# Kernel tuning notes

Hardware: AMD Instinct MI355X
Metric: run time of the kernel (lower is better)

## Reference

```python
import jax, jax.numpy as jnp
import numpy as np

B, S, D = 2, 2048, 2048
H, HK = 16, 4          # n_heads, n_kv_heads
DK = D // H            # 128
REP = H // HK


def setup_inputs() -> dict:
    key = jax.random.key(0)
    ks = jax.random.split(key, 9)
    x = jax.random.normal(ks[0], (B, S, D), dtype=jnp.float32)
    # RoPE tables: [max_seq_len, d_k/2]
    inv_freq = 1.0 / (10000.0 ** (jnp.arange(0, DK, 2, dtype=jnp.float32) / DK))
    t = jnp.arange(S, dtype=jnp.float32)
    freqs = jnp.outer(t, inv_freq)  # [S, DK/2]
    freqs_cos = jnp.cos(freqs)
    freqs_sin = jnp.sin(freqs)
    sc = 0.02
    return {
        "x": x,
        "freqs_cos": freqs_cos,
        "freqs_sin": freqs_sin,
        "wq_w": jax.random.normal(ks[1], (D, D), dtype=jnp.float32) * sc,
        "wq_b": jnp.zeros((D,), dtype=jnp.float32),
        "wk_w": jax.random.normal(ks[2], (HK * DK, D), dtype=jnp.float32) * sc,
        "wk_b": jnp.zeros((HK * DK,), dtype=jnp.float32),
        "wv_w": jax.random.normal(ks[3], (HK * DK, D), dtype=jnp.float32) * sc,
        "wv_b": jnp.zeros((HK * DK,), dtype=jnp.float32),
        "wo_w": jax.random.normal(ks[4], (D, D), dtype=jnp.float32) * sc,
        "wo_b": jnp.zeros((D,), dtype=jnp.float32),
    }


def _apply_rope(t, cos, sin):
    # t: [b, h, s, dk]; cos/sin: [1, 1, s, dk/2]; interleaved pairs (even=real, odd=imag)
    tr = t[..., 0::2]
    ti = t[..., 1::2]
    out_r = tr * cos - ti * sin
    out_i = tr * sin + ti * cos
    return jnp.stack([out_r, out_i], axis=-1).reshape(t.shape)


def reference(x, freqs_cos, freqs_sin, wq_w, wq_b, wk_w, wk_b, wv_w, wv_b, wo_w, wo_b):
    b, s, d = x.shape
    q = (x @ wq_w.T + wq_b).reshape(b, s, H, DK).transpose(0, 2, 1, 3)   # [b,H,s,dk]
    k = (x @ wk_w.T + wk_b).reshape(b, s, HK, DK).transpose(0, 2, 1, 3)  # [b,HK,s,dk]
    v = (x @ wv_w.T + wv_b).reshape(b, s, HK, DK).transpose(0, 2, 1, 3)

    cos = freqs_cos[:s][None, None]  # [1,1,s,dk/2]
    sin = freqs_sin[:s][None, None]
    q = _apply_rope(q, cos, sin)
    k = _apply_rope(k, cos, sin)

    # GQA: group q heads by kv head instead of materializing repeat_kv
    qg = q.reshape(b, HK, REP, s, DK)
    scores = jnp.einsum("bgrqd,bgkd->bgrqk", qg, k) / jnp.sqrt(jnp.float32(DK))
    causal = jnp.triu(jnp.full((s, s), -jnp.inf, dtype=scores.dtype), k=1)
    attn = jax.nn.softmax(scores + causal, axis=-1)  # dropout=0.0 -> no-op
    out = jnp.einsum("bgrqk,bgkd->bgrqd", attn, v)   # [b,HK,REP,s,dk]
    out = out.reshape(b, H, s, DK).transpose(0, 2, 1, 3).reshape(b, s, d)
    return out @ wo_w.T + wo_b
```

## Files before the change

### kernel.cpp

```cpp
#include <hip/hip_runtime.h>

#define BDIM 2
#define SDIM 2048
#define DDIM 2048
#define HQ 16
#define HKV 4
#define DKH 128
#define NKV 512
#define NQKV 3072
#define MROWS 4096

typedef __attribute__((ext_vector_type(8))) short bf16x8;
typedef __attribute__((ext_vector_type(4))) float f32x4;
typedef __attribute__((ext_vector_type(8))) unsigned short u16x8;
typedef __attribute__((ext_vector_type(4))) unsigned short u16x4;

#define AS1 __attribute__((address_space(1)))
#define AS3 __attribute__((address_space(3)))

__device__ __forceinline__ unsigned short f2bf(float f) {
    union { float f; unsigned int u; } v; v.f = f;
    unsigned int r = v.u + 0x7FFFu + ((v.u >> 16) & 1u);
    return (unsigned short)(r >> 16);
}
__device__ __forceinline__ float bf2f(unsigned short u) {
    union { unsigned int u; float f; } v; v.u = ((unsigned int)u) << 16;
    return v.f;
}
__device__ __forceinline__ unsigned int pack2bf(float a, float b) {
    return (unsigned int)f2bf(a) | ((unsigned int)f2bf(b) << 16);
}

#define NX   ((size_t)MROWS * DDIM)
#define NWQ  ((size_t)DDIM * DDIM)
#define NWKV ((size_t)NKV * DDIM)
#define CAST_BLOCKS 18432
__global__ void cast_all(const float* __restrict__ x, const float* __restrict__ wq,
                         const float* __restrict__ wk, const float* __restrict__ wv,
                         const float* __restrict__ wo, unsigned short* __restrict__ dst,
                         const float* __restrict__ qb, const float* __restrict__ kb,
                         const float* __restrict__ vb, float* __restrict__ b3) {
    if (blockIdx.x >= CAST_BLOCKS) {
        int i = (blockIdx.x - CAST_BLOCKS) * 256 + threadIdx.x;
        if (i < DDIM) b3[i] = qb[i];
        else if (i < DDIM + NKV) b3[i] = kb[i - DDIM];
        else if (i < NQKV) b3[i] = vb[i - DDIM - NKV];
        return;
    }
    size_t i = ((size_t)blockIdx.x * blockDim.x + threadIdx.x) * 4;
    const size_t N0 = NX, N1 = N0 + NWQ, N2 = N1 + NWKV, N3 = N2 + NWKV;
    const float* src; size_t off;
    if (i < N0)      { src = x;  off = i; }
    else if (i < N1) { src = wq; off = i - N0; }
    else if (i < N2) { src = wk; off = i - N1; }
    else if (i < N3) { src = wv; off = i - N2; }
    else             { src = wo; off = i - N3; }
    float4 v = *(const float4*)(src + off);
    u16x4 o;
    o[0] = f2bf(v.x); o[1] = f2bf(v.y); o[2] = f2bf(v.z); o[3] = f2bf(v.w);
    *(u16x4*)(dst + i) = o;
}

__global__ void rope_trans(unsigned short* __restrict__ buf,
                           const float* __restrict__ cosT, const float* __restrict__ sinT,
                           unsigned short* __restrict__ Vt, float qscale) {
    if (blockIdx.x < MROWS) {
        int r = blockIdx.x, pos = r & (SDIM - 1);
        int col0 = threadIdx.x * 8;
        unsigned short* p = buf + (size_t)r * NQKV + col0;
        int i0 = (col0 & 127) >> 1;
        float4 c4 = *(const float4*)(cosT + pos * 64 + i0);
        float4 s4 = *(const float4*)(sinT + pos * 64 + i0);
        float sc = (col0 < DDIM) ? qscale : 1.f;
        u16x8 v = *(const u16x8*)p;
        u16x8 o;
        float cc[4] = {c4.x, c4.y, c4.z, c4.w}, ss[4] = {s4.x, s4.y, s4.z, s4.w};
#pragma unroll
        for (int k = 0; k < 4; ++k) {
            float xr = bf2f(v[2 * k]), xi = bf2f(v[2 * k + 1]);
            o[2 * k]     = f2bf((xr * cc[k] - xi * ss[k]) * sc);
            o[2 * k + 1] = f2bf((xr * ss[k] + xi * cc[k]) * sc);
        }
        *(u16x8*)p = o;
    } else {
        __shared__ unsigned short T[32][33];
        if (threadIdx.x >= 256) return;
        int t = blockIdx.x - MROWS;
        int s0 = (t & 63) * 32, d0 = ((t >> 6) & 15) * 32, b = t >> 10;
        int c = threadIdx.x & 31, r4 = threadIdx.x >> 5;
        for (int rr = r4; rr < 32; rr += 8)
            T[rr][c] = buf[(size_t)(b * SDIM + s0 + rr) * NQKV + (DDIM + NKV) + d0 + c];
        __syncthreads();
        int cp = ((c & 0x0C) << 1) | ((c & 0x10) >> 2) | (c & 3);
        for (int rr = r4; rr < 32; rr += 8)
            Vt[(size_t)(b * NKV + d0 + rr) * SDIM + s0 + cp] = T[c][rr];
    }
}

template <int BF16OUT, int BM, int BN, int WM, int WN>
__global__ __launch_bounds__(512, 2) void gemm8(
    const unsigned short* __restrict__ A,
    const unsigned short* __restrict__ Bm,
    const float* __restrict__ bias,
    void* __restrict__ Cv,
    int pitch, int Kdim) {
    constexpr int NFRAG = BN / WN / 16;
    constexpr int AH = BM / 128;
    constexpr int BH = BN / 128;
    constexpr int AHR = BM / 2;
    constexpr int BHR = BN / 2;

    __shared__ unsigned short As[2][2][AHR * 64];
    __shared__ unsigned short Bs[2][2][BHR * 64];

    const int tid = threadIdx.x;
    const int lane = tid & 63;
    const int wid = tid >> 6;
    const int ml = lane & 15, quad = lane >> 4;
    const int wm = wid / WN, wn = wid % WN;
    const int bhf = wn / (WN / 2);
    const int brb = (wn % (WN / 2)) * (BN / WN);

    const int gx = gridDim.x;
    const int nwg = gx * gridDim.y;
    int w0 = blockIdx.y * gx + blockIdx.x;
    int wsw = (nwg & 7) ? w0 : ((w0 & 7) * (nwg >> 3) + (w0 >> 3));
    const int m0 = (wsw / gx) * BM, n0 = (wsw % gx) * BN;

    const int NT = Kdim >> 6;
    const int xr = ml & 7;

    const int sr = tid >> 3;
    const int sk = ((tid & 7) ^ (sr & 7)) * 8;
    const unsigned short* Ag0 = A + (size_t)(m0 + sr) * Kdim + sk;
    const unsigned short* Bg0 = Bm + (size_t)(n0 + sr) * Kdim + sk;

    f32x4 acc[8][NFRAG] = {};

#define STG_A(bf, hf, kt)                                                                       \
    do {                                                                                        \
        _Pragma("unroll")                                                                       \
        for (int ll = 0; ll < AH; ++ll)                                                         \
            __builtin_amdgcn_global_load_lds(                                                   \
                (const AS1 unsigned int*)(Ag0 + (size_t)((hf) * AHR + ll * 64) * Kdim + (kt)),  \
                (AS3 unsigned int*)(&As[bf][hf][ll * 4096 + tid * 8]), 16, 0, 0);               \
    } while (0)
#define STG_B(bf, hf, kt)                                                                       \
    do {                                                                                        \
        _Pragma("unroll")                                                                       \
        for (int ll = 0; ll < BH; ++ll)                                                         \
            __builtin_amdgcn_global_load_lds(                                                   \
                (const AS1 unsigned int*)(Bg0 + (size_t)((hf) * BHR + ll * 64) * Kdim + (kt)),  \
                (AS3 unsigned int*)(&Bs[bf][hf][ll * 4096 + tid * 8]), 16, 0, 0);               \
    } while (0)

    STG_B(0, 0, 0); STG_B(0, 1, 0);
    STG_A(0, 0, 0); STG_A(0, 1, 0);
    if (NT > 1) {
        STG_B(1, 0, 64); STG_B(1, 1, 64);
        if constexpr (BH == 1)      asm volatile("s_waitcnt vmcnt(2)" ::: "memory");
        else if constexpr (BH == 2) asm volatile("s_waitcnt vmcnt(4)" ::: "memory");
        else                        asm volatile("s_waitcnt vmcnt(6)" ::: "memory");
    } else {
        asm volatile("s_waitcnt vmcnt(0)" ::: "memory");
    }
    __builtin_amdgcn_s_barrier();

    for (int G = 0; G < NT; ++G) {
        const int cur = G & 1, nxt = cur ^ 1;
        const int ktA = (G + 1) * 64, ktB = (G + 2) * 64;
        const unsigned short* Bh = Bs[cur][bhf];

        bf16x8 bfr[NFRAG][2];
#pragma unroll
        for (int nj = 0; nj < NFRAG; ++nj)
#pragma unroll
            for (int kk = 0; kk < 2; ++kk)
                bfr[nj][kk] = *(const bf16x8*)&Bh[(brb + nj * 16 + ml) * 64 + ((kk * 4 + quad) ^ xr) * 8];

#pragma unroll
        for (int p = 0; p < 4; ++p) {
            bf16x8 af[2][2];
#pragma unroll
            for (int mi = 0; mi < 2; ++mi) {
                const int arow0 = wm * 128 + (p * 2 + mi) * 16;
                const int ahf = arow0 / AHR;
                const int arin = arow0 % AHR + ml;
#pragma unroll
                for (int kk = 0; kk < 2; ++kk)
                    af[mi][kk] = *(const bf16x8*)&As[cur][ahf][arin * 64 + ((kk * 4 + quad) ^ xr) * 8];
            }

            if (p == 0) {
                if (G + 1 < NT) { STG_A(nxt, 0, ktA); STG_A(nxt, 1, ktA); }
            } else if (p == 2) {
                if (G + 2 < NT) STG_B(cur, 0, ktB);
            } else if (p == 3) {
                if (G + 2 < NT) STG_B(cur, 1, ktB);
            }

            __builtin_amdgcn_s_barrier();
            __builtin_amdgcn_s_setprio(1);
#pragma unroll
            for (int kk = 0; kk < 2; ++kk)
#pragma unroll
                for (int mi = 0; mi < 2; ++mi)
#pragma unroll
                    for (int nj = 0; nj < NFRAG; ++nj)
                        acc[p * 2 + mi][nj] = __builtin_amdgcn_mfma_f32_16x16x32_bf16(
                            af[mi][kk], bfr[nj][kk], acc[p * 2 + mi][nj], 0, 0, 0);
            __builtin_amdgcn_s_setprio(0);
            if (p == 3) {
                if (G < NT - 2) {
                    if constexpr (BH == 1)      asm volatile("s_waitcnt vmcnt(2)" ::: "memory");
                    else if constexpr (BH == 2) asm volatile("s_waitcnt vmcnt(4)" ::: "memory");
                    else                        asm volatile("s_waitcnt vmcnt(6)" ::: "memory");
                } else if (G == NT - 2) {
                    asm volatile("s_waitcnt vmcnt(0)" ::: "memory");
                }
            }
            __builtin_amdgcn_s_barrier();
        }
    }
#undef STG_A
#undef STG_B

#pragma unroll
    for (int nj = 0; nj < NFRAG; ++nj) {
        const int col = n0 + wn * (BN / WN) + nj * 16 + ml;
        const float bj = bias[col];
#pragma unroll
        for (int mi = 0; mi < 8; ++mi) {
            const int row0 = m0 + wm * 128 + mi * 16 + quad * 4;
#pragma unroll
            for (int rr = 0; rr < 4; ++rr) {
                float v = acc[mi][nj][rr] + bj;
                if (BF16OUT)
                    ((unsigned short*)Cv)[(size_t)(row0 + rr) * pitch + col] = f2bf(v);
                else
                    ((float*)Cv)[(size_t)(row0 + rr) * pitch + col] = v;
            }
        }
    }
}

__global__ __launch_bounds__(256, 2) void attn_fwd(
    const unsigned short* __restrict__ Qp,
    const unsigned short* __restrict__ Kp,
    const unsigned short* __restrict__ Vt,
    unsigned short* __restrict__ O) {
    const int l = blockIdx.x;
    const int j = l & 15;
    const int h = (l >> 4) & 15;
    const int b = l >> 8;
    const int g = h >> 2;
    const int jh = 31 - j;
    const int tid = threadIdx.x;
    const int w = tid >> 6, lane = tid & 63;
    const int ml = lane & 15, quad = lane >> 4;
    const int rsub = lane >> 2, seg = lane & 3;
    const int pr = w >> 1;
    const int wsub = w & 1;

    __shared__ unsigned short Ks[2][4 * 64 * 32];
    __shared__ unsigned short Vs[2][2 * 128 * 32];

    int myqt = pr ? j : jh;
    int q0 = myqt * 64 + wsub * 32;

    bf16x8 aq[2][4];
    auto load_q = [&](int qt) {
#pragma unroll
        for (int g2 = 0; g2 < 2; ++g2) {
            const size_t qrow = (size_t)(b * SDIM + qt * 64 + wsub * 32 + g2 * 16 + ml);
#pragma unroll
            for (int kc = 0; kc < 4; ++kc)
                aq[g2][kc] = *(const bf16x8*)(Qp + qrow * NQKV + h * DKH + kc * 32 + quad * 8);
        }
    };
    load_q(myqt);

    f32x4 o_acc[2][8] = {};
    float l_acc[2] = {0.f, 0.f};

    auto store_out = [&](int qt) {
#pragma unroll
        for (int g2 = 0; g2 < 2; ++g2) {
            float lt = l_acc[g2];
            lt += __shfl_xor(lt, 16);
            lt += __shfl_xor(lt, 32);
            float inv = 1.f / lt;
            size_t rowbase = (size_t)(b * SDIM + qt * 64 + wsub * 32 + g2 * 16 + ml) * DDIM + h * DKH + quad * 4;
#pragma unroll
            for (int dt = 0; dt < 8; ++dt) {
                u16x4 ov;
#pragma unroll
                for (int r = 0; r < 4; ++r)
                    ov[r] = f2bf(o_acc[g2][dt][r] * inv);
                *(u16x4*)(O + rowbase + dt * 16) = ov;
            }
        }
    };

    for (int it = 0; it < 17; ++it) {
        int kt;
        if (pr == 0)       kt = it;
        else if (it <= j)  kt = it;
        else if (it <= 15) kt = 16 + it - j;
        else               kt = -1;

        __syncthreads();
        if (kt >= 0) {
            const int kb = kt * 64;
#pragma unroll
            for (int kc = 0; kc < 4; ++kc)
#pragma unroll
                for (int rh = 0; rh < 2; ++rh)
                    __builtin_amdgcn_global_load_lds(
                        (const AS1 unsigned int*)(Kp + (size_t)(b * SDIM + kb + rh * 32 + wsub * 16 + rsub) * NQKV + g * DKH + kc * 32 + seg * 8),
                        (AS3 unsigned int*)(&Ks[pr][kc * 2048 + rh * 1024 + wsub * 512 + lane * 8]), 16, 0, 0);
#pragma unroll
            for (int c = 0; c < 8; ++c) {
                int u = wsub * 8 + c, kc2 = u >> 3, rg = u & 7;
                __builtin_amdgcn_global_load_lds(
                    (const AS1 unsigned int*)(Vt + (size_t)(b * NKV + g * DKH + rg * 16 + rsub) * SDIM + kb + kc2 * 32 + seg * 8),
                    (AS3 unsigned int*)(&Vs[pr][u * 512 + lane * 8]), 16, 0, 0);
            }
        }
        __syncthreads();

        if (pr == 1 && it == j + 1) {
            store_out(j);
            myqt = jh; q0 = myqt * 64 + wsub * 32;
            load_q(jh);
#pragma unroll
            for (int g2 = 0; g2 < 2; ++g2) {
                l_acc[g2] = 0.f;
#pragma unroll
                for (int dt = 0; dt < 8; ++dt) o_acc[g2][dt] = (f32x4){0.f, 0.f, 0.f, 0.f};
            }
        }

        if (kt >= 0) {
            const int kb = kt * 64;
            __builtin_amdgcn_s_setprio(1);
            f32x4 st[2][4];
#pragma unroll
            for (int t = 0; t < 4; ++t) {
                bf16x8 ak[4];
#pragma unroll
                for (int kc = 0; kc < 4; ++kc)
                    ak[kc] = *(const bf16x8*)&Ks[pr][kc * 2048 + (t * 16 + ml) * 32 + quad * 8];
#pragma unroll
                for (int g2 = 0; g2 < 2; ++g2) {
                    f32x4 sc = {};
#pragma unroll
                    for (int kc = 0; kc < 4; ++kc)
                        sc = __builtin_amdgcn_mfma_f32_16x16x32_bf16(ak[kc], aq[g2][kc], sc, 0, 0, 0);
                    st[g2][t] = sc;
                }
            }

            if (kb + 63 > q0) {
#pragma unroll
                for (int g2 = 0; g2 < 2; ++g2) {
                    int qg = q0 + g2 * 16 + ml;
#pragma unroll
                    for (int t = 0; t < 4; ++t) {
                        int kvb = kb + t * 16 + quad * 4;
#pragma unroll
                        for (int r = 0; r < 4; ++r)
                            if (kvb + r > qg) st[g2][t][r] = -INFINITY;
                    }
                }
            }

            unsigned int pk[2][4][2];
#pragma unroll
            for (int g2 = 0; g2 < 2; ++g2) {
#pragma unroll
                for (int t = 0; t < 4; ++t) {
                    float p0 = __expf(st[g2][t][0] - 20.f);
                    float p1 = __expf(st[g2][t][1] - 20.f);
                    float p2 = __expf(st[g2][t][2] - 20.f);
                    float p3 = __expf(st[g2][t][3] - 20.f);
                    l_acc[g2] += (p0 + p1) + (p2 + p3);
                    pk[g2][t][0] = pack2bf(p0, p1);
                    pk[g2][t][1] = pack2bf(p2, p3);
                }
            }

#pragma unroll
            for (int c = 0; c < 2; ++c) {
                union { unsigned int u[4]; bf16x8 v; } pb[2];
#pragma unroll
                for (int g2 = 0; g2 < 2; ++g2) {
                    pb[g2].u[0] = pk[g2][2 * c][0];     pb[g2].u[1] = pk[g2][2 * c][1];
                    pb[g2].u[2] = pk[g2][2 * c + 1][0]; pb[g2].u[3] = pk[g2][2 * c + 1][1];
                }
#pragma unroll
                for (int dt = 0; dt < 8; ++dt) {
                    bf16x8 av = *(const bf16x8*)&Vs[pr][c * 4096 + (dt * 16 + ml) * 32 + quad * 8];
                    o_acc[0][dt] = __builtin_amdgcn_mfma_f32_16x16x32_bf16(av, pb[0].v, o_acc[0][dt], 0, 0, 0);
                    o_acc[1][dt] = __builtin_amdgcn_mfma_f32_16x16x32_bf16(av, pb[1].v, o_acc[1][dt], 0, 0, 0);
                }
            }
            __builtin_amdgcn_s_setprio(0);
        }
    }

    __syncthreads();
    float* Fo = (float*)&Ks[0][0];
    float* Fl = (float*)&Vs[0][0];
    if (pr == 0) {
#pragma unroll
        for (int g2 = 0; g2 < 2; ++g2) {
            Fl[(g2 * 2 + wsub) * 64 + lane] = l_acc[g2];
#pragma unroll
            for (int dt = 0; dt < 8; ++dt)
                *(f32x4*)&Fo[(g2 * 8 + dt) * 512 + wsub * 256 + lane * 4] = o_acc[g2][dt];
        }
    }
    __syncthreads();
    if (pr == 1) {
#pragma unroll
        for (int g2 = 0; g2 < 2; ++g2) {
            l_acc[g2] += Fl[(g2 * 2 + wsub) * 64 + lane];
#pragma unroll
            for (int dt = 0; dt < 8; ++dt) {
                f32x4 pa = *(const f32x4*)&Fo[(g2 * 8 + dt) * 512 + wsub * 256 + lane * 4];
#pragma unroll
                for (int r = 0; r < 4; ++r) o_acc[g2][dt][r] += pa[r];
            }
        }
        store_out(jh);
    }
}

extern "C" void kernel_launch(void* const* d_in, const int* in_sizes, int n_in,
                              void* d_out, int out_size, void* d_ws, size_t ws_size,
                              hipStream_t stream) {
    const float* x    = (const float*)d_in[0];
    const float* fcos = (const float*)d_in[1];
    const float* fsin = (const float*)d_in[2];
    const float* wq_w = (const float*)d_in[3];
    const float* wq_b = (const float*)d_in[4];
    const float* wk_w = (const float*)d_in[5];
    const float* wk_b = (const float*)d_in[6];
    const float* wv_w = (const float*)d_in[7];
    const float* wv_b = (const float*)d_in[8];
    const float* wo_w = (const float*)d_in[9];
    const float* wo_b = (const float*)d_in[10];
    float* out = (float*)d_out;

    char* ws = (char*)d_ws;
    size_t off = 0;
    auto alloc = [&](size_t bytes) {
        char* p = ws + off;
        off += (bytes + 255) & ~(size_t)255;
        return p;
    };
    unsigned short* xb  = (unsigned short*)alloc(NX * 2);
    unsigned short* W3  = (unsigned short*)alloc((size_t)NQKV * DDIM * 2);
    unsigned short* wob = (unsigned short*)alloc(NWQ * 2);
    float* b3           = (float*)alloc((size_t)NQKV * 4);
    unsigned short* qkv = (unsigned short*)alloc((size_t)MROWS * NQKV * 2);
    unsigned short* Vt  = (unsigned short*)alloc((size_t)BDIM * NKV * SDIM * 2);
    unsigned short* att = (unsigned short*)alloc((size_t)MROWS * DDIM * 2);

    cast_all<<<dim3(CAST_BLOCKS + 12), dim3(256), 0, stream>>>(
        x, wq_w, wk_w, wv_w, wo_w, xb, wq_b, wk_b, wv_b, b3);

    gemm8<1, 128, 384, 1, 8><<<dim3(NQKV / 384, MROWS / 128), 512, 0, stream>>>(
        xb, W3, b3, qkv, NQKV, DDIM);

    const float scale = 0.08838834764831845f;
    rope_trans<<<dim3(MROWS + 2048), dim3(320), 0, stream>>>(qkv, fcos, fsin, Vt, scale);

    attn_fwd<<<dim3(512), dim3(256), 0, stream>>>(qkv, qkv + DDIM, Vt, att);

    gemm8<0, 256, 128, 2, 4><<<dim3(DDIM / 128, MROWS / 256), 512, 0, stream>>>(
        att, wob, wo_b, out, DDIM, DDIM);
}
```

Baseline: 302.9 us.

## Restructure GEMM main loop into single-phase compute with fewer barriers

Replaces the four-phase per-tile inner loop, which interleaved A-fragment loads, staged global-to-LDS copies and MFMA bursts with two barriers per phase, with a single phase per K-tile. All A fragments are loaded up front, every MFMA is issued in one burst, and the B prefetch and vmcnt wait are grouped after one barrier. Sched barriers pin the ordering. The row-fragment count is generalized to BM/WM/16. This cuts barrier count and scheduling stalls, but raises register pressure from holding all A fragments and reduces overlap of copies with MFMA work.

```diff
diff --git a/kernel.cpp b/kernel.cpp
--- a/kernel.cpp
+++ b/kernel.cpp
@@ -104,6 +104,7 @@
     const float* __restrict__ bias,
     void* __restrict__ Cv,
     int pitch, int Kdim) {
+    constexpr int MF = BM / WM / 16;
     constexpr int NFRAG = BN / WN / 16;
     constexpr int AH = BM / 128;
     constexpr int BH = BN / 128;
@@ -135,7 +136,7 @@
     const unsigned short* Ag0 = A + (size_t)(m0 + sr) * Kdim + sk;
     const unsigned short* Bg0 = Bm + (size_t)(n0 + sr) * Kdim + sk;
 
-    f32x4 acc[8][NFRAG] = {};
+    f32x4 acc[MF][NFRAG] = {};
 
 #define STG_A(bf, hf, kt)                                                                       \
     do {                                                                                        \
@@ -153,18 +154,23 @@
                 (const AS1 unsigned int*)(Bg0 + (size_t)((hf) * BHR + ll * 64) * Kdim + (kt)),  \
                 (AS3 unsigned int*)(&Bs[bf][hf][ll * 4096 + tid * 8]), 16, 0, 0);               \
     } while (0)
+#define WAIT_VM_STEADY()                                                                        \
+    do {                                                                                        \
+        if constexpr (BH == 1)      asm volatile("s_waitcnt vmcnt(2)" ::: "memory");            \
+        else if constexpr (BH == 2) asm volatile("s_waitcnt vmcnt(4)" ::: "memory");            \
+        else                        asm volatile("s_waitcnt vmcnt(6)" ::: "memory");            \
+    } while (0)
 
     STG_B(0, 0, 0); STG_B(0, 1, 0);
     STG_A(0, 0, 0); STG_A(0, 1, 0);
     if (NT > 1) {
         STG_B(1, 0, 64); STG_B(1, 1, 64);
-        if constexpr (BH == 1)      asm volatile("s_waitcnt vmcnt(2)" ::: "memory");
-        else if constexpr (BH == 2) asm volatile("s_waitcnt vmcnt(4)" ::: "memory");
-        else                        asm volatile("s_waitcnt vmcnt(6)" ::: "memory");
+        WAIT_VM_STEADY();
     } else {
         asm volatile("s_waitcnt vmcnt(0)" ::: "memory");
     }
     __builtin_amdgcn_s_barrier();
+    __builtin_amdgcn_sched_barrier(0);
 
     for (int G = 0; G < NT; ++G) {
         const int cur = G & 1, nxt = cur ^ 1;
@@ -178,63 +184,55 @@
             for (int kk = 0; kk < 2; ++kk)
                 bfr[nj][kk] = *(const bf16x8*)&Bh[(brb + nj * 16 + ml) * 64 + ((kk * 4 + quad) ^ xr) * 8];
 
-#pragma unroll
-        for (int p = 0; p < 4; ++p) {
-            bf16x8 af[2][2];
-#pragma unroll
-            for (int mi = 0; mi < 2; ++mi) {
-                const int arow0 = wm * 128 + (p * 2 + mi) * 16;
-                const int ahf = arow0 / AHR;
-                const int arin = arow0 % AHR + ml;
-#pragma unroll
-                for (int kk = 0; kk < 2; ++kk)
-                    af[mi][kk] = *(const bf16x8*)&As[cur][ahf][arin * 64 + ((kk * 4 + quad) ^ xr) * 8];
-            }
-
-            if (p == 0) {
-                if (G + 1 < NT) { STG_A(nxt, 0, ktA); STG_A(nxt, 1, ktA); }
-            } else if (p == 2) {
-                if (G + 2 < NT) STG_B(cur, 0, ktB);
-            } else if (p == 3) {
-                if (G + 2 < NT) STG_B(cur, 1, ktB);
-            }
-
-            __builtin_amdgcn_s_barrier();
-            __builtin_amdgcn_s_setprio(1);
+        bf16x8 af[MF][2];
+#pragma unroll
+        for (int mf = 0; mf < MF; ++mf) {
+            const int arow0 = wm * (BM / WM) + mf * 16;
+            const int ahf = arow0 / AHR;
+            const int arin = arow0 % AHR + ml;
 #pragma unroll
             for (int kk = 0; kk < 2; ++kk)
-#pragma unroll
-                for (int mi = 0; mi < 2; ++mi)
-#pragma unroll
-                    for (int nj = 0; nj < NFRAG; ++nj)
-                        acc[p * 2 + mi][nj] = __builtin_amdgcn_mfma_f32_16x16x32_bf16(
-                            af[mi][kk], bfr[nj][kk], acc[p * 2 + mi][nj], 0, 0, 0);
-            __builtin_amdgcn_s_setprio(0);
-            if (p == 3) {
-                if (G < NT - 2) {
-                    if constexpr (BH == 1)      asm volatile("s_waitcnt vmcnt(2)" ::: "memory");
-                    else if constexpr (BH == 2) asm volatile("s_waitcnt vmcnt(4)" ::: "memory");
-                    else                        asm volatile("s_waitcnt vmcnt(6)" ::: "memory");
-                } else if (G == NT - 2) {
-                    asm volatile("s_waitcnt vmcnt(0)" ::: "memory");
-                }
-            }
-            __builtin_amdgcn_s_barrier();
-        }
+                af[mf][kk] = *(const bf16x8*)&As[cur][ahf][arin * 64 + ((kk * 4 + quad) ^ xr) * 8];
+        }
+
+        if (G + 1 < NT) { STG_A(nxt, 0, ktA); STG_A(nxt, 1, ktA); }
+
+        __builtin_amdgcn_s_setprio(1);
+#pragma unroll
+        for (int kk = 0; kk < 2; ++kk)
+#pragma unroll
+            for (int mf = 0; mf < MF; ++mf)
+#pragma unroll
+                for (int nj = 0; nj < NFRAG; ++nj)
+                    acc[mf][nj] = __builtin_amdgcn_mfma_f32_16x16x32_bf16(
+                        af[mf][kk], bfr[nj][kk], acc[mf][nj], 0, 0, 0);
+        __builtin_amdgcn_s_setprio(0);
+
+        asm volatile("s_waitcnt lgkmcnt(0)" ::: "memory");
+        __builtin_amdgcn_sched_barrier(0);
+        __builtin_amdgcn_s_barrier();
+
+        if (G + 2 < NT) { STG_B(cur, 0, ktB); STG_B(cur, 1, ktB); }
+        if (G < NT - 2)       { WAIT_VM_STEADY(); }
+        else if (G == NT - 2) { asm volatile("s_waitcnt vmcnt(0)" ::: "memory"); }
+        __builtin_amdgcn_sched_barrier(0);
+        __builtin_amdgcn_s_barrier();
+        __builtin_amdgcn_sched_barrier(0);
     }
 #undef STG_A
 #undef STG_B
+#undef WAIT_VM_STEADY
 
 #pragma unroll
     for (int nj = 0; nj < NFRAG; ++nj) {
         const int col = n0 + wn * (BN / WN) + nj * 16 + ml;
         const float bj = bias[col];
 #pragma unroll
-        for (int mi = 0; mi < 8; ++mi) {
-            const int row0 = m0 + wm * 128 + mi * 16 + quad * 4;
+        for (int mf = 0; mf < MF; ++mf) {
+            const int row0 = m0 + wm * (BM / WM) + mf * 16 + quad * 4;
 #pragma unroll
             for (int rr = 0; rr < 4; ++rr) {
-                float v = acc[mi][nj][rr] + bj;
+                float v = acc[mf][nj][rr] + bj;
                 if (BF16OUT)
                     ((unsigned short*)Cv)[(size_t)(row0 + rr) * pitch + col] = f2bf(v);
                 else
```

After: 294.7 us. 2.7% less time.
